# Kernel optimization log

Hardware: AMD Instinct MI355X
Metric: run time of the kernel (lower is better)

The kernel has to match this reference:

```python
import jax, jax.numpy as jnp
import numpy as np

N_ENT = 40000
N_REL2 = 500      # num_rel * 2
E_DIR = 200000
E_2HOP = 50000
D_IN = 128        # entity/relation init dim
D_EMB = 256       # embed_dim
N_HEADS = 4
N_HID = D_EMB // N_HEADS  # 64
LRELU_ALPHA = 0.2
BN_EPS = 1e-5


def setup_inputs() -> dict:
    key = jax.random.key(0)
    ks = jax.random.split(key, 13)
    s = 0.1  # weight init scale
    return {
        "edge_index": jax.random.randint(ks[0], (2, E_DIR), 0, N_ENT),
        "edge_type": jax.random.randint(ks[1], (E_DIR,), 0, N_REL2),
        "indices_2hop": jax.random.randint(ks[2], (E_2HOP, 4), 0, N_REL2),
        "init_embed": jax.random.normal(ks[3], (N_ENT, D_IN), jnp.float32) * s,
        "init_rel": jax.random.normal(ks[4], (N_REL2, D_IN), jnp.float32) * s,
        "W_heads": jax.random.normal(ks[5], (N_HEADS, 2 * D_IN + D_IN, N_HID), jnp.float32) * s,
        "a_heads": jax.random.normal(ks[6], (N_HEADS, N_HID, 1), jnp.float32) * s,
        "gat_W": jax.random.normal(ks[7], (D_IN, D_EMB), jnp.float32) * s,
        "out_W": jax.random.normal(ks[8], (2 * D_EMB + D_EMB, D_EMB), jnp.float32) * s,
        "out_a": jax.random.normal(ks[9], (D_EMB, 1), jnp.float32) * s,
        "W_entities": jax.random.normal(ks[10], (D_IN, D_EMB), jnp.float32) * s,
        "bn_gamma": jnp.ones((D_EMB,), jnp.float32),
        "bn_beta": jnp.zeros((D_EMB,), jnp.float32),
    }


def segment_softmax(logits, idx, num_seg):
    # sparse softmax grouped by idx (PyG-style): subtract per-segment max, exp, normalize
    m = jax.ops.segment_max(logits, idx, num_segments=num_seg)
    e = jnp.exp(logits - m[idx])
    s = jax.ops.segment_sum(e, idx, num_segments=num_seg)
    return e / (s[idx] + 1e-16)


def reference(edge_index, edge_type, indices_2hop, init_embed, init_rel,
              W_heads, a_heads, gat_W, out_W, out_a, W_entities, bn_gamma, bn_beta):
    n = init_embed.shape[0]
    # build full edge list: flipped direct edges + 2-hop edges
    edge_nhop = jnp.stack([indices_2hop[:, 3], indices_2hop[:, 0]])  # [2, E2]
    ei = jnp.concatenate([edge_index[::-1], edge_nhop], axis=1)      # [2, Etot]
    row, col = ei[0], ei[1]
    t0, t1 = indices_2hop[:, 1], indices_2hop[:, 2]

    # first-layer edge relation embeddings
    edge_embed = jnp.concatenate([init_rel[edge_type], init_rel[t0] + init_rel[t1]], axis=0)
    feat = jnp.concatenate([init_embed[row], init_embed[col], edge_embed], axis=1)  # [Etot, 3*D_IN]

    def head(W, a):
        eh = feat @ W                                     # [Etot, N_HID]
        logit = jax.nn.leaky_relu((eh @ a)[:, 0], LRELU_ALPHA)
        alpha = segment_softmax(logit, row, n)
        agg = jax.ops.segment_sum(alpha[:, None] * eh, row, num_segments=n)
        return jax.nn.elu(agg)                            # concat=True -> elu

    x = jax.vmap(head)(W_heads, a_heads)                  # [H, N, N_HID]
    x = jnp.transpose(x, (1, 0, 2)).reshape(n, -1)        # [N, H*N_HID]

    r = init_rel @ gat_W                                  # [R2, D_EMB]
    edge_embed2 = jnp.concatenate([r[edge_type], r[t0] + r[t1]], axis=0)
    feat2 = jnp.concatenate([x[row], x[col], edge_embed2], axis=1)  # [Etot, 3*D_EMB]
    eh2 = feat2 @ out_W                                   # [Etot, D_EMB]
    logit2 = jax.nn.leaky_relu((eh2 @ out_a)[:, 0], LRELU_ALPHA)
    alpha2 = segment_softmax(logit2, row, n)
    out = jax.ops.segment_sum(alpha2[:, None] * eh2, row, num_segments=n)
    x = jax.nn.elu(out)                                   # elu applied in GAT.forward

    x = x + init_embed @ W_entities
    # BatchNorm1d (training-mode batch stats, biased variance)
    mu = jnp.mean(x, axis=0)
    var = jnp.var(x, axis=0)
    x = (x - mu) / jnp.sqrt(var + BN_EPS) * bn_gamma + bn_beta
    return x, r
```

## Files before the change

kernel.cpp:

```cpp
#include <hip/hip_runtime.h>
#include <hip/hip_bf16.h>
#include <math.h>

#define N_ENT 40000
#define N_REL 500
#define E_DIR 200000
#define E_2HOP 50000
#define E_TOT 250000
#define D_IN 128
#define D_EMB 256
#define LRELU 0.2f
#define BN_EPS 1e-5f
#define NB_SCAN 157
#define NB_EDGE 977
#define N_HEAVY 500
#define DEG_SPLIT 32

typedef __hip_bfloat16 bf16;
typedef __attribute__((ext_vector_type(8))) short short8;
typedef __attribute__((ext_vector_type(4))) float float4v;

__device__ __forceinline__ float b2f(bf16 v){ return __bfloat162float(v); }
__device__ __forceinline__ float bitsf(unsigned int u){ return __builtin_bit_cast(float, u); }
__device__ __forceinline__ unsigned short bbits(float v){ return __builtin_bit_cast(unsigned short, __float2bfloat16(v)); }

__device__ __forceinline__ int e_row(int e, const int* ei, const int* i2){
  return (e < E_DIR) ? ei[E_DIR + e] : i2[(e - E_DIR)*4 + 3];
}

__global__ void prep_hist(const float* __restrict__ Wh, const float* __restrict__ ow,
                          const float* __restrict__ we, const float* __restrict__ emb,
                          bf16* __restrict__ WAp, bf16* __restrict__ WBp, bf16* __restrict__ WEp,
                          bf16* __restrict__ OWp0, bf16* __restrict__ OWp1, float* __restrict__ WC,
                          bf16* __restrict__ embb,
                          const int* __restrict__ ei, const int* __restrict__ i2, int* __restrict__ cnt){
  const int HS = 384*64;
  int b = blockIdx.x, tid = threadIdx.x;
  if (b < NB_EDGE){
    int e = b*256 + tid;
    if (e < E_TOT) atomicAdd(&cnt[e_row(e, ei, i2)], 1);
    return;
  }
  b -= NB_EDGE;
  if (b >= 240){
    int i = (b - 240)*256 + tid;
    embb[i] = __float2bfloat16(emb[i]);
    return;
  }
  if (b < 112){
    int seg, base;
    if      (b < 16){ seg = 0; base = 0; }
    else if (b < 32){ seg = 1; base = 16; }
    else if (b < 48){ seg = 2; base = 32; }
    else if (b < 80){ seg = 3; base = 48; }
    else            { seg = 4; base = 80; }
    int idx = (b - base)*256 + tid;
    int lane = idx & 63, nt = (idx >> 6) & 15, kc = idx >> 10;
    int quad = lane >> 4, l16 = lane & 15;
    int col = nt*16 + l16;
    int kbase = kc*32 + quad*8;
    bf16* dst = (seg==0?WAp : seg==1?WBp : seg==2?WEp : seg==3?OWp0 : OWp1) + (size_t)idx*8;
    #pragma unroll
    for (int j = 0; j < 8; j++){
      int k = kbase + j;
      float v;
      if      (seg == 0) v = Wh[(col>>6)*HS + k*64 + (col&63)];
      else if (seg == 1) v = Wh[(col>>6)*HS + (k+128)*64 + (col&63)];
      else if (seg == 2) v = we[(size_t)k*256 + col];
      else if (seg == 3) v = ow[(size_t)k*256 + col];
      else               v = ow[(size_t)(k+256)*256 + col];
      dst[j] = __float2bfloat16(v);
    }
  } else {
    int idx = (b - 112)*256 + tid;
    int k = idx >> 8, col = idx & 255;
    WC[idx] = Wh[(col>>6)*HS + (k+256)*64 + (col&63)];
  }
}

__global__ void scan_bsum(const int* __restrict__ cnt, int* __restrict__ bsum){
  int i = blockIdx.x*256 + threadIdx.x;
  int v = (i < N_ENT) ? cnt[i] : 0;
  int lane = threadIdx.x & 63, w = threadIdx.x >> 6;
  int s = v;
  #pragma unroll
  for (int o = 32; o >= 1; o >>= 1) s += __shfl_xor(s, o, 64);
  __shared__ int ws[4];
  if (lane == 0) ws[w] = s;
  __syncthreads();
  if (threadIdx.x == 0) bsum[blockIdx.x] = ws[0]+ws[1]+ws[2]+ws[3];
}

__global__ __launch_bounds__(256) void scan_final2(const int* __restrict__ cnt,
    const int* __restrict__ bsum, int* __restrict__ off){
  __shared__ int boffs[NB_SCAN];
  __shared__ int ws4[4];
  __shared__ int ws2[4];
  __shared__ int totals;
  int t = threadIdx.x;
  int lane = t & 63, w = t >> 6;
  {
    int v = (t < NB_SCAN) ? bsum[t] : 0;
    int s = v;
    #pragma unroll
    for (int o = 1; o < 64; o <<= 1){ int n = __shfl_up(s, o, 64); if (lane >= o) s += n; }
    if (lane == 63) ws4[w] = s;
    __syncthreads();
    int add = 0;
    for (int k = 0; k < w; k++) add += ws4[k];
    int incl = s + add;
    if (t < NB_SCAN) boffs[t] = incl - v;
    if (t == NB_SCAN-1) totals = incl;
  }
  __syncthreads();
  int i = blockIdx.x*256 + t;
  int v = (i < N_ENT) ? cnt[i] : 0;
  int s = v;
  #pragma unroll
  for (int o = 1; o < 64; o <<= 1){ int n = __shfl_up(s, o, 64); if (lane >= o) s += n; }
  if (lane == 63) ws2[w] = s;
  __syncthreads();
  int add = boffs[blockIdx.x];
  for (int k = 0; k < w; k++) add += ws2[k];
  if (i < N_ENT) off[i] = add + s - v;
  if (blockIdx.x == 0 && t == 0) off[N_ENT] = totals;
}

__device__ __forceinline__ void mfma_panel(const short* __restrict__ A,
    const short* __restrict__ Bp, bf16* __restrict__ C, int K,
    const float* __restrict__ avec, float* __restrict__ Sout, int dmode,
    int bx, int half){
  int w = threadIdx.x >> 6, lane = threadIdx.x & 63;
  int quad = lane >> 4, l16 = lane & 15;
  int rm = bx*64 + w*16;
  int arow = rm + l16;
  float4v acc[8];
  #pragma unroll
  for (int nt = 0; nt < 8; nt++) acc[nt] = (float4v){0.f,0.f,0.f,0.f};
  int nkc = K >> 5;
  const short8* Ap = (const short8*)(A + (size_t)arow*K);
  const short8* Bv = (const short8*)Bp + half*512 + lane;
  short8 a_cur = Ap[quad];
  for (int kc = 0; kc < nkc; kc++){
    int kn = (kc + 1 < nkc) ? kc + 1 : kc;
    short8 a_nxt = Ap[kn*4 + quad];
    const short8* bp = Bv + (size_t)kc*1024;
    short8 b[4];
    #pragma unroll
    for (int nt = 0; nt < 4; nt++) b[nt] = bp[nt*64];
    #pragma unroll
    for (int nt = 0; nt < 4; nt++)
      acc[nt] = __builtin_amdgcn_mfma_f32_16x16x32_bf16(a_cur, b[nt], acc[nt], 0, 0, 0);
    #pragma unroll
    for (int nt = 0; nt < 4; nt++) b[nt] = bp[(nt+4)*64];
    #pragma unroll
    for (int nt = 0; nt < 4; nt++)
      acc[nt+4] = __builtin_amdgcn_mfma_f32_16x16x32_bf16(a_cur, b[nt], acc[nt+4], 0, 0, 0);
    a_cur = a_nxt;
  }
  #pragma unroll
  for (int nt = 0; nt < 8; nt++){
    int col = (half*8 + nt)*16 + l16;
    #pragma unroll
    for (int r = 0; r < 4; r++)
      C[(size_t)(rm + quad*4 + r)*256 + col] = __float2bfloat16(acc[nt][r]);
  }
  if (Sout){
    if (dmode == 0){
      #pragma unroll
      for (int hl = 0; hl < 2; hl++){
        float pr[4] = {0.f,0.f,0.f,0.f};
        #pragma unroll
        for (int ntl = 0; ntl < 4; ntl++){
          int ln = hl*4 + ntl;
          float av = avec[(half*8 + ln)*16 + l16];
          #pragma unroll
          for (int r = 0; r < 4; r++) pr[r] += acc[ln][r]*av;
        }
        #pragma unroll
        for (int m = 8; m >= 1; m >>= 1)
          #pragma unroll
          for (int r = 0; r < 4; r++) pr[r] += __shfl_xor(pr[r], m, 64);
        if (l16 == 0){
          #pragma unroll
          for (int r = 0; r < 4; r++)
            Sout[(rm + quad*4 + r)*4 + half*2 + hl] = pr[r];
        }
      }
    } else {
      float pr[4] = {0.f,0.f,0.f,0.f};
      #pragma unroll
      for (int ln = 0; ln < 8; ln++){
        float av = avec[(half*8 + ln)*16 + l16];
        #pragma unroll
        for (int r = 0; r < 4; r++) pr[r] += acc[ln][r]*av;
      }
      #pragma unroll
      for (int m = 8; m >= 1; m >>= 1)
        #pragma unroll
        for (int r = 0; r < 4; r++) pr[r] += __shfl_xor(pr[r], m, 64);
      if (l16 == 0){
        #pragma unroll
        for (int r = 0; r < 4; r++) atomicAdd(&Sout[rm + quad*4 + r], pr[r]);
      }
    }
  }
}

__device__ __forceinline__ void gemm64_body(const float* __restrict__ A,
    const float* __restrict__ B, float* __restrict__ C, bf16* __restrict__ Cb,
    int M, int K, const float* __restrict__ av, float* __restrict__ So, int mode,
    int bxx, int byy, char* smem){
  const int N = 256;
  float (*As)[65] = (float (*)[65])smem;
  float (*Bsf)[65] = (float (*)[65])(smem + 16*65*sizeof(float));
  int bm = bxx * 64, bn = byy * 64;
  int tid = threadIdx.x;
  int tx = tid & 15, ty = tid >> 4;
  float acc[4][4] = {};
  for (int k0 = 0; k0 < K; k0 += 16){
    #pragma unroll
    for (int j = 0; j < 4; j++){
      int idx = tid + j*256;
      int m = idx >> 4, kk = idx & 15;
      int gm = bm + m;
      float v = 0.f;
      if (gm < M) v = A[(size_t)gm*K + k0 + kk];
      As[kk][m] = v;
    }
    #pragma unroll
    for (int j = 0; j < 4; j++){
      int idx = tid + j*256;
      int kk = idx >> 6, n = idx & 63;
      Bsf[kk][n] = B[(size_t)(k0+kk)*N + bn + n];
    }
    __syncthreads();
    #pragma unroll
    for (int kk = 0; kk < 16; kk++){
      float a[4], b[4];
      #pragma unroll
      for (int i = 0; i < 4; i++) a[i] = As[kk][ty*4+i];
      #pragma unroll
      for (int j = 0; j < 4; j++) b[j] = Bsf[kk][tx*4+j];
      #pragma unroll
      for (int i = 0; i < 4; i++)
        #pragma unroll
        for (int j = 0; j < 4; j++) acc[i][j] += a[i]*b[j];
    }
    __syncthreads();
  }
  if (Cb){
    #pragma unroll
    for (int i = 0; i < 4; i++){
      int gm = bm + ty*4 + i;
      if (gm >= M) continue;
      #pragma unroll
      for (int j = 0; j < 4; j++)
        Cb[(size_t)gm*N + bn + tx*4 + j] = __float2bfloat16(acc[i][j]);
    }
  } else {
    #pragma unroll
    for (int i = 0; i < 4; i++){
      int gm = bm + ty*4 + i;
      if (gm >= M) continue;
      #pragma unroll
      for (int j = 0; j < 4; j++)
        C[(size_t)gm*N + bn + tx*4 + j] = acc[i][j];
    }
  }
  if (mode != 2){
    float pr[4];
    #pragma unroll
    for (int i = 0; i < 4; i++){
      float p = 0.f;
      #pragma unroll
      for (int j = 0; j < 4; j++) p += acc[i][j]*av[bn + tx*4 + j];
      pr[i] = p;
    }
    #pragma unroll
    for (int m = 8; m >= 1; m >>= 1)
      #pragma unroll
      for (int i = 0; i < 4; i++) pr[i] += __shfl_xor(pr[i], m, 64);
    if (tx == 0){
      #pragma unroll
      for (int i = 0; i < 4; i++){
        int gm = bm + ty*4 + i;
        if (gm < M){
          if (mode == 0) So[gm*4 + byy] = pr[i];
          else atomicAdd(&So[gm], pr[i]);
        }
      }
    }
  }
}

__device__ __forceinline__ void scatter_body(const int* __restrict__ ei, const int* __restrict__ et,
    const int* __restrict__ i2, const int* __restrict__ off,
    int* __restrict__ cur, int4* __restrict__ EIDX, int blk){
  int e = blk*256 + threadIdx.x;
  if (e >= E_TOT) return;
  int r = e_row(e, ei, i2);
  int p = atomicAdd(&cur[r], 1);
  int d = off[r] + p;
  int4 v;
  if (e < E_DIR){ v.x = ei[e]; v.y = et[e]; v.z = -1; }
  else { int q = (e - E_DIR)*4; v.x = i2[q]; v.y = i2[q+1]; v.z = i2[q+2]; }
  v.w = r;
  EIDX[d] = v;
}

__global__ __launch_bounds__(256, 4) void mega1(
    const short* __restrict__ embb, const short* __restrict__ WAp, const short* __restrict__ WBp,
    const short* __restrict__ WEp, bf16* __restrict__ P1, bf16* __restrict__ P2, bf16* __restrict__ EP,
    const float* __restrict__ ah, float* __restrict__ S1, float* __restrict__ S2,
    const float* __restrict__ rel, const float* __restrict__ WC, const float* __restrict__ gw,
    float* __restrict__ RF, float* __restrict__ SRm, bf16* __restrict__ PRb,
    const int* __restrict__ ei, const int* __restrict__ et, const int* __restrict__ i2,
    const int* __restrict__ off, int* __restrict__ cur, int4* __restrict__ EIDX, int useEP){
  __shared__ char smem[8704];
  int y = blockIdx.y, x = blockIdx.x;
  if (x < 1250){
    if (y == 2 && !useEP) return;
    const short* B = y==0 ? WAp : (y==1 ? WBp : WEp);
    bf16* C = y==0 ? P1 : (y==1 ? P2 : EP);
    float* S = y==0 ? S1 : (y==1 ? S2 : nullptr);
    mfma_panel(embb, B, C, 128, ah, S, 0, x >> 1, x & 1);
    return;
  }
  int r = x - 1250;
  if (y == 0){
    if (r < 64){
      int z = r >> 5, rr = r & 31, by = rr >> 3, bx = rr & 7;
      if (z == 0) gemm64_body(rel, WC, nullptr, PRb, N_REL, 128, ah, SRm, 0, bx, by, smem);
      else        gemm64_body(rel, gw, RF, nullptr, N_REL, 128, nullptr, nullptr, 2, bx, by, smem);
    }
  } else if (y == 1){
    if (r < NB_EDGE) scatter_body(ei, et, i2, off, cur, EIDX, r);
  }
}

__global__ __launch_bounds__(256, 4) void mega2(
    const short* __restrict__ X1s, const short* __restrict__ OWp0, const short* __restrict__ OWp1,
    bf16* __restrict__ Q1, bf16* __restrict__ Q2, const float* __restrict__ oa,
    float* __restrict__ S1B, float* __restrict__ S2B,
    const float* __restrict__ RF, const float* __restrict__ owB, float* __restrict__ SRB,
    bf16* __restrict__ QRb){
  __shared__ char smem[8704];
  int y = blockIdx.y, x = blockIdx.x;
  if (x < 1250){
    mfma_panel(X1s, y==0 ? OWp0 : OWp1, y==0 ? Q1 : Q2, 256, oa,
               y==0 ? S1B : S2B, 1, x >> 1, x & 1);
    return;
  }
  int r = x - 1250;
  if (y == 0 && r < 32){
    int by = r >> 3, bx = r & 7;
    gemm64_body(RF, owB, nullptr, QRb, N_REL, 256, oa, SRB, 1, bx, by, smem);
  }
}

__global__ void gemm64_acc(const float* __restrict__ A, const float* __restrict__ B,
                           float* __restrict__ C, int M, int K){
  const int N = 256;
  __shared__ float As[16][65];
  __shared__ float Bs[16][65];
  int bm = blockIdx.x * 64, bn = blockIdx.y * 64;
  int tid = threadIdx.x;
  int tx = tid & 15, ty = tid >> 4;
  float acc[4][4] = {};
  for (int k0 = 0; k0 < K; k0 += 16){
    #pragma unroll
    for (int j = 0; j < 4; j++){
      int idx = tid + j*256;
      int m = idx >> 4, kk = idx & 15;
      int gm = bm + m;
      float v = 0.f;
      if (gm < M) v = A[(size_t)gm*K + k0 + kk];
      As[kk][m] = v;
    }
    #pragma unroll
    for (int j = 0; j < 4; j++){
      int idx = tid + j*256;
      int kk = idx >> 6, n = idx & 63;
      Bs[kk][n] = B[(size_t)(k0+kk)*N + bn + n];
    }
    __syncthreads();
    #pragma unroll
    for (int kk = 0; kk < 16; kk++){
      float a[4], b[4];
      #pragma unroll
      for (int i = 0; i < 4; i++) a[i] = As[kk][ty*4+i];
      #pragma unroll
      for (int j = 0; j < 4; j++) b[j] = Bs[kk][tx*4+j];
      #pragma unroll
      for (int i = 0; i < 4; i++)
        #pragma unroll
        for (int j = 0; j < 4; j++) acc[i][j] += a[i]*b[j];
    }
    __syncthreads();
  }
  #pragma unroll
  for (int i = 0; i < 4; i++){
    int gm = bm + ty*4 + i;
    if (gm >= M) continue;
    #pragma unroll
    for (int j = 0; j < 4; j++){
      size_t o = (size_t)gm*N + bn + tx*4 + j;
      C[o] += acc[i][j];
    }
  }
}

__global__ __launch_bounds__(256) void sm1f(const int* __restrict__ off, const int4* __restrict__ EIDX,
    const float* __restrict__ s1, const float* __restrict__ s2, const float* __restrict__ sR,
    float* __restrict__ L1, float* __restrict__ AS1, float* __restrict__ IV1){
  if (blockIdx.x < N_HEAVY){
    int i = blockIdx.x;
    int st = off[i], en = off[i+1];
    if (en - st <= DEG_SPLIT) return;
    int h = threadIdx.x >> 6, lane = threadIdx.x & 63;
    float* Lh = L1 + (size_t)h*E_TOT;
    float si = s1[i*4 + h];
    float mx = -1e30f;
    for (int t = st + lane; t < en; t += 64){
      int4 e = EIDX[t];
      float v = si + s2[e.x*4+h] + sR[e.y*4+h];
      if (e.z >= 0) v += sR[e.z*4+h];
      v = (v >= 0.f) ? v : LRELU*v;
      Lh[t] = v;
      mx = fmaxf(mx, v);
    }
    #pragma unroll
    for (int o = 32; o >= 1; o >>= 1) mx = fmaxf(mx, __shfl_xor(mx, o, 64));
    float sm = 0.f;
    for (int t = st + lane; t < en; t += 64){
      float ev = __expf(Lh[t] - mx); Lh[t] = ev; sm += ev;
    }
    #pragma unroll
    for (int o = 32; o >= 1; o >>= 1) sm += __shfl_xor(sm, o, 64);
    float inv = 1.f/(sm + 1e-16f);
    if (lane == 0){ AS1[i*4+h] = sm*inv; IV1[i*4+h] = inv; }
    return;
  }
  int wid = threadIdx.x >> 6, lane = threadIdx.x & 63;
  int i = (blockIdx.x - N_HEAVY)*4 + wid;
  if (i >= N_ENT) return;
  int st = off[i], en = off[i+1];
  if (i < N_HEAVY && en - st > DEG_SPLIT) return;
  int hf = lane >> 4, l16 = lane & 15;
  float* Lh = L1 + (size_t)hf*E_TOT;
  float si = s1[i*4 + hf];
  if (en - st > 2*16){
    float mx = -1e30f;
    for (int t = st + l16; t < en; t += 16){
      int4 e = EIDX[t];
      float v = si + s2[e.x*4+hf] + sR[e.y*4+hf];
      if (e.z >= 0) v += sR[e.z*4+hf];
      v = (v >= 0.f) ? v : LRELU*v;
      Lh[t] = v; mx = fmaxf(mx, v);
    }
    #pragma unroll
    for (int o = 8; o >= 1; o >>= 1) mx = fmaxf(mx, __shfl_xor(mx, o, 64));
    float sm = 0.f;
    for (int t = st + l16; t < en; t += 16){
      float ev = __expf(Lh[t] - mx); Lh[t] = ev; sm += ev;
    }
    #pragma unroll
    for (int o = 8; o >= 1; o >>= 1) sm += __shfl_xor(sm, o, 64);
    float inv = 1.f/(sm + 1e-16f);
    if (l16 == 0){ AS1[i*4+hf] = sm*inv; IV1[i*4+hf] = inv; }
    return;
  }
  int t0 = st + l16, t1 = t0 + 16;
  float v0 = -1e30f, v1 = -1e30f;
  if (t0 < en){
    int4 e = EIDX[t0];
    float v = si + s2[e.x*4+hf] + sR[e.y*4+hf];
    if (e.z >= 0) v += sR[e.z*4+hf];
    v0 = (v >= 0.f) ? v : LRELU*v;
  }
  if (t1 < en){
    int4 e = EIDX[t1];
    float v = si + s2[e.x*4+hf] + sR[e.y*4+hf];
    if (e.z >= 0) v += sR[e.z*4+hf];
    v1 = (v >= 0.f) ? v : LRELU*v;
  }
  float mx = fmaxf(v0, v1);
  #pragma unroll
  for (int o = 8; o >= 1; o >>= 1) mx = fmaxf(mx, __shfl_xor(mx, o, 64));
  float sm = 0.f;
  if (t0 < en){ float ev = __expf(v0 - mx); Lh[t0] = ev; sm += ev; }
  if (t1 < en){ float ev = __expf(v1 - mx); Lh[t1] = ev; sm += ev; }
  #pragma unroll
  for (int o = 8; o >= 1; o >>= 1) sm += __shfl_xor(sm, o, 64);
  float inv = 1.f/(sm + 1e-16f);
  if (l16 == 0){ AS1[i*4+hf] = sm*inv; IV1[i*4+hf] = inv; }
}

__global__ __launch_bounds__(256) void sm2f(const int* __restrict__ off, const int4* __restrict__ EIDX,
    const float* __restrict__ s1, const float* __restrict__ s2, const float* __restrict__ sR,
    float* __restrict__ L2, float* __restrict__ AS2, float* __restrict__ IV2){
  __shared__ float wsm[4], wss[4];
  if (blockIdx.x < N_HEAVY){
    int i = blockIdx.x;
    int st = off[i], en = off[i+1];
    if (en - st <= DEG_SPLIT) return;
    int tid = threadIdx.x, w = tid >> 6, lane = tid & 63;
    float si = s1[i];
    float mx = -1e30f;
    for (int t = st + tid; t < en; t += 256){
      int4 e = EIDX[t];
// ... 304 lines not shown
  int wid = threadIdx.x >> 6, lane = threadIdx.x & 63;
  int i = (blockIdx.x - N_HEAVY)*4 + wid;
  if (i >= N_ENT) return;
  int st = off[i], en = off[i+1];
  if (i < N_HEAVY && en - st > DEG_SPLIT) return;
  int f0 = lane*4;
  size_t ob = (size_t)i*256 + f0;
  float ep0=0.f, ep1=0.f, ep2=0.f, ep3=0.f;
  if (EP){
    uint2 ue = *(const uint2*)(EP + ob);
    ep0 = bitsf(ue.x << 16); ep1 = bitsf(ue.x & 0xffff0000u);
    ep2 = bitsf(ue.y << 16); ep3 = bitsf(ue.y & 0xffff0000u);
  }
  if (st == en){
    *(float4*)(X2 + ob) = (float4){ep0, ep1, ep2, ep3};
    return;
  }
  float a0=0,a1=0,a2=0,a3=0;
  int t = st;
  int n4 = st + ((en - st) & ~3);
  for (; t < n4; t += 4){
    int4 e[4]; float wv[4]; uint2 u[4]; uint2 rr[4];
    #pragma unroll
    for (int k = 0; k < 4; k++){ e[k] = EIDX[t+k]; wv[k] = W2[t+k]; }
    #pragma unroll
    for (int k = 0; k < 4; k++){
      u[k] = *(const uint2*)(Q2 + (size_t)e[k].x*256 + f0);
      rr[k] = *(const uint2*)(QRm + (size_t)e[k].y*256 + f0);
    }
    float rf[4][4];
    #pragma unroll
    for (int k = 0; k < 4; k++){ UNPK(rr[k], rf[k][0], rf[k][1], rf[k][2], rf[k][3]) }
    #pragma unroll
    for (int k = 0; k < 4; k++){
      if (e[k].z >= 0){
        uint2 s = *(const uint2*)(QRm + (size_t)e[k].z*256 + f0);
        float s0,s1,s2,s3; UNPK(s, s0,s1,s2,s3)
        rf[k][0] += s0; rf[k][1] += s1; rf[k][2] += s2; rf[k][3] += s3;
      }
    }
    #pragma unroll
    for (int k = 0; k < 4; k++){
      a0 += wv[k]*(bitsf(u[k].x << 16) + rf[k][0]);
      a1 += wv[k]*(bitsf(u[k].x & 0xffff0000u) + rf[k][1]);
      a2 += wv[k]*(bitsf(u[k].y << 16) + rf[k][2]);
      a3 += wv[k]*(bitsf(u[k].y & 0xffff0000u) + rf[k][3]);
    }
  }
  for (; t < en; t++){
    float w = W2[t];
    int4 e = EIDX[t];
    uint2 u = *(const uint2*)(Q2 + (size_t)e.x*256 + f0);
    uint2 rr = *(const uint2*)(QRm + (size_t)e.y*256 + f0);
    float r0,r1,r2,r3; UNPK(rr, r0,r1,r2,r3)
    if (e.z >= 0){
      uint2 s = *(const uint2*)(QRm + (size_t)e.z*256 + f0);
      float s0,s1,s2,s3; UNPK(s, s0,s1,s2,s3)
      r0 += s0; r1 += s1; r2 += s2; r3 += s3;
    }
    a0 += w*(bitsf(u.x << 16) + r0);
    a1 += w*(bitsf(u.x & 0xffff0000u) + r1);
    a2 += w*(bitsf(u.y << 16) + r2);
    a3 += w*(bitsf(u.y & 0xffff0000u) + r3);
  }
  float iv = IV2[i];
  a0 *= iv; a1 *= iv; a2 *= iv; a3 *= iv;
  float as = AS2[i];
  uint2 uq = *(const uint2*)(Q1 + ob);
  a0 += as*bitsf(uq.x << 16);
  a1 += as*bitsf(uq.x & 0xffff0000u);
  a2 += as*bitsf(uq.y << 16);
  a3 += as*bitsf(uq.y & 0xffff0000u);
  a0 = ((a0 > 0.f) ? a0 : __expf(a0)-1.f) + ep0;
  a1 = ((a1 > 0.f) ? a1 : __expf(a1)-1.f) + ep1;
  a2 = ((a2 > 0.f) ? a2 : __expf(a2)-1.f) + ep2;
  a3 = ((a3 > 0.f) ? a3 : __expf(a3)-1.f) + ep3;
  *(float4*)(X2 + ob) = (float4){a0, a1, a2, a3};
}

__global__ void bn_reduce(const float* __restrict__ X, float* __restrict__ sums, float* __restrict__ sq){
  int ch = threadIdx.x;
  float s = 0.f, q = 0.f;
  for (int r = blockIdx.x; r < N_ENT; r += gridDim.x){
    float v = X[(size_t)r*256 + ch];
    s += v; q += v*v;
  }
  atomicAdd(&sums[ch], s);
  atomicAdd(&sq[ch], q);
}

__global__ void bn_final_r(float* __restrict__ X, const float* __restrict__ sums, const float* __restrict__ sq,
                           const float* __restrict__ gamma, const float* __restrict__ beta,
                           const float* __restrict__ RF, float* __restrict__ out_r){
  int b = blockIdx.x;
  if (b < 40000){
    int idx = b*256 + threadIdx.x;
    int ch = idx & 255;
    const float invn = 1.f/(float)N_ENT;
    float mean = sums[ch] * invn;
    float var  = fmaxf(sq[ch] * invn - mean*mean, 0.f);
    X[idx] = (X[idx] - mean) * rsqrtf(var + BN_EPS) * gamma[ch] + beta[ch];
  } else {
    int idx = (b - 40000)*256 + threadIdx.x;
    out_r[idx] = RF[idx];
  }
}

extern "C" void kernel_launch(void* const* d_in, const int* in_sizes, int n_in,
                              void* d_out, int out_size, void* d_ws, size_t ws_size,
                              hipStream_t stream){
  const int*   ei  = (const int*)d_in[0];
  const int*   et  = (const int*)d_in[1];
  const int*   i2  = (const int*)d_in[2];
  const float* emb = (const float*)d_in[3];
  const float* rel = (const float*)d_in[4];
  const float* Wh  = (const float*)d_in[5];
  const float* ah  = (const float*)d_in[6];
  const float* gw  = (const float*)d_in[7];
  const float* ow  = (const float*)d_in[8];
  const float* oa  = (const float*)d_in[9];
  const float* we  = (const float*)d_in[10];
  const float* gma = (const float*)d_in[11];
  const float* bta = (const float*)d_in[12];
  float* out = (float*)d_out;

  char* ws = (char*)d_ws;
  size_t o = 0;
  auto alloc = [&](size_t bytes)->char*{
    char* p = ws + o; o = (o + bytes + 255) & ~(size_t)255; return p;
  };
  bf16*  P1  = (bf16*)alloc(20480000);
  bf16*  P2  = (bf16*)alloc(20480000);
  bf16*  PRb = (bf16*)alloc(256000);
  bf16*  QRb = (bf16*)alloc(256000);
  float* RF  = (float*)alloc(512000);
  float* WC  = (float*)alloc(131072);
  bf16*  WAp = (bf16*)alloc(65536);
  bf16*  WBp = (bf16*)alloc(65536);
  bf16*  WEp = (bf16*)alloc(65536);
  bf16*  OWp0= (bf16*)alloc(131072);
  bf16*  OWp1= (bf16*)alloc(131072);
  float* S1  = (float*)alloc(640000);
  float* S2  = (float*)alloc(640000);
  float* SRm = (float*)alloc(8192);
  float* S1B = (float*)alloc(160000);
  float* S2B = (float*)alloc(160000);
  int*   CNT = (int*)alloc(160000);
  int*   CUR = (int*)alloc(160000);
  float* SRB = (float*)alloc(2048);
  float* BNS = (float*)alloc(1024);
  float* BNQ = (float*)alloc(1024);
  int*   OFF = (int*)alloc(160016);
  int*   BSUM= (int*)alloc(1024);
  int4*  EIDX= (int4*)alloc(4000000);
  float* L1  = (float*)alloc(4000000);
  float* L2  = (float*)alloc(1000000);
  float* AS1 = (float*)alloc(640000);
  float* AS2 = (float*)alloc(160000);
  float* IV1 = (float*)alloc(640000);
  float* IV2 = (float*)alloc(160000);
  size_t base_end = o;
  bool useEP = (ws_size >= base_end + 20480256 + 512);
  bf16* EP = nullptr;
  if (useEP) EP = (bf16*)alloc(20480000);
  bf16* X1b  = (bf16*)out;
  bf16* embb = (bf16*)((char*)out + 20480000);
  float* X2 = out;
  (void)in_sizes; (void)n_in; (void)out_size;

  hipMemsetAsync(S1B, 0, 644096, stream);

  prep_hist<<<NB_EDGE + 20240, 256, 0, stream>>>(Wh, ow, we, emb,
      WAp, WBp, WEp, OWp0, OWp1, WC, embb, ei, i2, CNT);

  scan_bsum<<<NB_SCAN, 256, 0, stream>>>(CNT, BSUM);
  scan_final2<<<NB_SCAN, 256, 0, stream>>>(CNT, BSUM, OFF);

  mega1<<<dim3(1250 + NB_EDGE, 3), 256, 0, stream>>>(
      (const short*)embb, (const short*)WAp, (const short*)WBp, (const short*)WEp,
      P1, P2, EP, ah, S1, S2,
      rel, WC, gw, RF, SRm, PRb,
      ei, et, i2, OFF, CUR, EIDX, useEP ? 1 : 0);

  sm1f<<<N_HEAVY + N_ENT/4, 256, 0, stream>>>(OFF, EIDX, S1, S2, SRm, L1, AS1, IV1);
  agg1<<<N_HEAVY + N_ENT/4, 256, 0, stream>>>(OFF, EIDX, L1, AS1, IV1, P1, P2, PRb, X1b);

  mega2<<<dim3(1250 + 32, 2), 256, 0, stream>>>(
      (const short*)X1b, (const short*)OWp0, (const short*)OWp1,
      P1, P2, oa, S1B, S2B, RF, ow + 131072, SRB, QRb);

  sm2f<<<N_HEAVY + N_ENT/4, 256, 0, stream>>>(OFF, EIDX, S1B, S2B, SRB, L2, AS2, IV2);
  agg2<<<N_HEAVY + N_ENT/4, 256, 0, stream>>>(OFF, EIDX, L2, AS2, IV2, P1, P2, QRb, EP, X2);

  if (!useEP)
    gemm64_acc<<<dim3((N_ENT+63)/64, 4), 256, 0, stream>>>(emb, we, X2, N_ENT, 128);

  bn_reduce<<<1024, 256, 0, stream>>>(X2, BNS, BNQ);
  bn_final_r<<<40500, 256, 0, stream>>>(X2, BNS, BNQ, gma, bta, RF, out + (size_t)N_ENT*256);
}
```

Before: 401.3 us.

## Make MFMA GEMM panels persistent with weight slices staged in LDS

Replaces the per-tile MFMA panel with a persistent kernel body. Each block loads its weight column slice into 32KB of shared memory once, using global_load_lds, then loops over row tiles with a stride, so B is no longer re-read from global memory for every tile. The launch grids of mega1 and mega2 are flattened to 1D and the column split is regrouped: mega2 now uses 4 quarter-width slices with K=256. The larger LDS footprint lowers achievable occupancy, and A rows are still streamed from global memory.

Result: slower. 463.5 us (+15.5%).

```diff
diff --git a/kernel.cpp b/kernel.cpp
--- a/kernel.cpp
+++ b/kernel.cpp
@@ -15,6 +15,9 @@
 #define NB_EDGE 977
 #define N_HEAVY 500
 #define DEG_SPLIT 32
+#define N_TILES 625
+#define BPU1 208
+#define BPU2 160
 
 typedef __hip_bfloat16 bf16;
 typedef __attribute__((ext_vector_type(8))) short short8;
@@ -23,6 +26,12 @@
 __device__ __forceinline__ float b2f(bf16 v){ return __bfloat162float(v); }
 __device__ __forceinline__ float bitsf(unsigned int u){ return __builtin_bit_cast(float, u); }
 __device__ __forceinline__ unsigned short bbits(float v){ return __builtin_bit_cast(unsigned short, __float2bfloat16(v)); }
+
+typedef const __attribute__((address_space(1))) void* gptr_t;
+typedef __attribute__((address_space(3))) void* lptr_t;
+__device__ __forceinline__ void gload_lds16(const void* g, void* l){
+  __builtin_amdgcn_global_load_lds((gptr_t)g, (lptr_t)l, 16, 0, 0);
+}
 
 __device__ __forceinline__ int e_row(int e, const int* ei, const int* i2){
   return (e < E_DIR) ? ei[E_DIR + e] : i2[(e - E_DIR)*4 + 3];
@@ -126,56 +135,99 @@
   if (blockIdx.x == 0 && t == 0) off[N_ENT] = totals;
 }
 
-__device__ __forceinline__ void mfma_panel(const short* __restrict__ A,
-    const short* __restrict__ Bp, bf16* __restrict__ C, int K,
+template<int NKC, int NTL>
+__device__ __forceinline__ void mfma_persist(const short* __restrict__ A,
+    const short* __restrict__ Bp, bf16* __restrict__ C,
     const float* __restrict__ avec, float* __restrict__ Sout, int dmode,
-    int bx, int half){
-  int w = threadIdx.x >> 6, lane = threadIdx.x & 63;
+    int nt0, int tile0, int stride, char* smem){
+  const int CPB8 = NTL*64;
+  int tid = threadIdx.x, w = tid >> 6, lane = tid & 63;
   int quad = lane >> 4, l16 = lane & 15;
-  int rm = bx*64 + w*16;
-  int arow = rm + l16;
-  float4v acc[8];
-  #pragma unroll
-  for (int nt = 0; nt < 8; nt++) acc[nt] = (float4v){0.f,0.f,0.f,0.f};
-  int nkc = K >> 5;
-  const short8* Ap = (const short8*)(A + (size_t)arow*K);
-  const short8* Bv = (const short8*)Bp + half*512 + lane;
-  short8 a_cur = Ap[quad];
-  for (int kc = 0; kc < nkc; kc++){
-    int kn = (kc + 1 < nkc) ? kc + 1 : kc;
-    short8 a_nxt = Ap[kn*4 + quad];
-    const short8* bp = Bv + (size_t)kc*1024;
-    short8 b[4];
-    #pragma unroll
-    for (int nt = 0; nt < 4; nt++) b[nt] = bp[nt*64];
-    #pragma unroll
-    for (int nt = 0; nt < 4; nt++)
-      acc[nt] = __builtin_amdgcn_mfma_f32_16x16x32_bf16(a_cur, b[nt], acc[nt], 0, 0, 0);
-    #pragma unroll
-    for (int nt = 0; nt < 4; nt++) b[nt] = bp[(nt+4)*64];
-    #pragma unroll
-    for (int nt = 0; nt < 4; nt++)
-      acc[nt+4] = __builtin_amdgcn_mfma_f32_16x16x32_bf16(a_cur, b[nt], acc[nt+4], 0, 0, 0);
-    a_cur = a_nxt;
-  }
-  #pragma unroll
-  for (int nt = 0; nt < 8; nt++){
-    int col = (half*8 + nt)*16 + l16;
-    #pragma unroll
-    for (int r = 0; r < 4; r++)
-      C[(size_t)(rm + quad*4 + r)*256 + col] = __float2bfloat16(acc[nt][r]);
-  }
-  if (Sout){
-    if (dmode == 0){
-      #pragma unroll
-      for (int hl = 0; hl < 2; hl++){
+  {
+    const short8* Bv = (const short8*)Bp;
+    short8* Bw = (short8*)smem;
+    #pragma unroll
+    for (int kc = 0; kc < NKC; kc++){
+      #pragma unroll
+      for (int s = 0; s < CPB8; s += 256){
+        int dstBase = kc*CPB8 + s + w*64;
+        size_t srcBase = (size_t)kc*1024 + nt0*64 + s + w*64;
+        gload_lds16((const void*)(Bv + srcBase + lane), (void*)(Bw + dstBase));
+      }
+    }
+  }
+  __syncthreads();
+  const short8* Bs = (const short8*)smem;
+  for (int t = tile0; t < N_TILES; t += stride){
+    int rm = t*64 + w*16;
+    int arow = rm + l16;
+    const short8* Ap = (const short8*)(A + (size_t)arow*(NKC*32));
+    short8 a[NKC];
+    #pragma unroll
+    for (int kc = 0; kc < NKC; kc++) a[kc] = Ap[kc*4 + quad];
+    float4v acc[NTL];
+    #pragma unroll
+    for (int n = 0; n < NTL; n++) acc[n] = (float4v){0.f,0.f,0.f,0.f};
+    #pragma unroll
+    for (int kc = 0; kc < NKC; kc++){
+      const short8* bp = Bs + kc*CPB8 + lane;
+      if (NTL == 8){
+        short8 b[4];
+        #pragma unroll
+        for (int n = 0; n < 4; n++) b[n] = bp[n*64];
+        #pragma unroll
+        for (int n = 0; n < 4; n++)
+          acc[n] = __builtin_amdgcn_mfma_f32_16x16x32_bf16(a[kc], b[n], acc[n], 0, 0, 0);
+        #pragma unroll
+        for (int n = 0; n < 4; n++) b[n] = bp[(n+4)*64];
+        #pragma unroll
+        for (int n = 0; n < 4; n++)
+          acc[n+4] = __builtin_amdgcn_mfma_f32_16x16x32_bf16(a[kc], b[n], acc[n+4], 0, 0, 0);
+      } else {
+        short8 b[NTL];
+        #pragma unroll
+        for (int n = 0; n < NTL; n++) b[n] = bp[n*64];
+        #pragma unroll
+        for (int n = 0; n < NTL; n++)
+          acc[n] = __builtin_amdgcn_mfma_f32_16x16x32_bf16(a[kc], b[n], acc[n], 0, 0, 0);
+      }
+    }
+    #pragma unroll
+    for (int n = 0; n < NTL; n++){
+      int col = (nt0 + n)*16 + l16;
+      #pragma unroll
+      for (int r = 0; r < 4; r++)
+        C[(size_t)(rm + quad*4 + r)*256 + col] = __float2bfloat16(acc[n][r]);
+    }
+    if (Sout){
+      if (dmode == 0){
+        #pragma unroll
+        for (int hl = 0; hl < 2; hl++){
+          float pr[4] = {0.f,0.f,0.f,0.f};
+          #pragma unroll
+          for (int n = 0; n < 4; n++){
+            float av = avec[(nt0 + hl*4 + n)*16 + l16];
+            #pragma unroll
+            for (int r = 0; r < 4; r++) pr[r] += acc[hl*4+n][r]*av;
+          }
+          #pragma unroll
+          for (int m = 8; m >= 1; m >>= 1)
+            #pragma unroll
+            for (int r = 0; r < 4; r++) pr[r] += __shfl_xor(pr[r], m, 64);
+          if (l16 == 0){
+            int head = (nt0 >> 2) + hl;
+            #pragma unroll
+            for (int r = 0; r < 4; r++)
+              Sout[(rm + quad*4 + r)*4 + head] = pr[r];
+          }
+        }
+      } else {
         float pr[4] = {0.f,0.f,0.f,0.f};
         #pragma unroll
-        for (int ntl = 0; ntl < 4; ntl++){
-          int ln = hl*4 + ntl;
-          float av = avec[(half*8 + ln)*16 + l16];
+        for (int n = 0; n < NTL; n++){
+          float av = avec[(nt0 + n)*16 + l16];
           #pragma unroll
-          for (int r = 0; r < 4; r++) pr[r] += acc[ln][r]*av;
+          for (int r = 0; r < 4; r++) pr[r] += acc[n][r]*av;
         }
         #pragma unroll
         for (int m = 8; m >= 1; m >>= 1)
@@ -183,25 +235,8 @@
           for (int r = 0; r < 4; r++) pr[r] += __shfl_xor(pr[r], m, 64);
         if (l16 == 0){
           #pragma unroll
-          for (int r = 0; r < 4; r++)
-            Sout[(rm + quad*4 + r)*4 + half*2 + hl] = pr[r];
+          for (int r = 0; r < 4; r++) atomicAdd(&Sout[rm + quad*4 + r], pr[r]);
         }
-      }
-    } else {
-      float pr[4] = {0.f,0.f,0.f,0.f};
-      #pragma unroll
-      for (int ln = 0; ln < 8; ln++){
-        float av = avec[(half*8 + ln)*16 + l16];
-        #pragma unroll
-        for (int r = 0; r < 4; r++) pr[r] += acc[ln][r]*av;
-      }
-      #pragma unroll
-      for (int m = 8; m >= 1; m >>= 1)
-        #pragma unroll
-        for (int r = 0; r < 4; r++) pr[r] += __shfl_xor(pr[r], m, 64);
-      if (l16 == 0){
-        #pragma unroll
-        for (int r = 0; r < 4; r++) atomicAdd(&Sout[rm + quad*4 + r], pr[r]);
       }
     }
   }
@@ -317,26 +352,27 @@
     float* __restrict__ RF, float* __restrict__ SRm, bf16* __restrict__ PRb,
     const int* __restrict__ ei, const int* __restrict__ et, const int* __restrict__ i2,
     const int* __restrict__ off, int* __restrict__ cur, int4* __restrict__ EIDX, int useEP){
-  __shared__ char smem[8704];
-  int y = blockIdx.y, x = blockIdx.x;
-  if (x < 1250){
-    if (y == 2 && !useEP) return;
-    const short* B = y==0 ? WAp : (y==1 ? WBp : WEp);
-    bf16* C = y==0 ? P1 : (y==1 ? P2 : EP);
-    float* S = y==0 ? S1 : (y==1 ? S2 : nullptr);
-    mfma_panel(embb, B, C, 128, ah, S, 0, x >> 1, x & 1);
-    return;
-  }
-  int r = x - 1250;
-  if (y == 0){
-    if (r < 64){
-      int z = r >> 5, rr = r & 31, by = rr >> 3, bx = rr & 7;
-      if (z == 0) gemm64_body(rel, WC, nullptr, PRb, N_REL, 128, ah, SRm, 0, bx, by, smem);
-      else        gemm64_body(rel, gw, RF, nullptr, N_REL, 128, nullptr, nullptr, 2, bx, by, smem);
-    }
-  } else if (y == 1){
-    if (r < NB_EDGE) scatter_body(ei, et, i2, off, cur, EIDX, r);
-  }
+  __shared__ char smem[32768];
+  int x = blockIdx.x;
+  if (x < 6*BPU1){
+    int u = x / BPU1;
+    int p = u >> 1, half = u & 1;
+    if (p == 2 && !useEP) return;
+    const short* B = p==0 ? WAp : (p==1 ? WBp : WEp);
+    bf16* C = p==0 ? P1 : (p==1 ? P2 : EP);
+    float* S = p==0 ? S1 : (p==1 ? S2 : nullptr);
+    mfma_persist<4,8>(embb, B, C, ah, S, 0, half*8, x % BPU1, BPU1, smem);
+    return;
+  }
+  int r = x - 6*BPU1;
+  if (r < 64){
+    int z = r >> 5, rr = r & 31, by = rr >> 3, bx = rr & 7;
+    if (z == 0) gemm64_body(rel, WC, nullptr, PRb, N_REL, 128, ah, SRm, 0, bx, by, smem);
+    else        gemm64_body(rel, gw, RF, nullptr, N_REL, 128, nullptr, nullptr, 2, bx, by, smem);
+    return;
+  }
+  r -= 64;
+  if (r < NB_EDGE) scatter_body(ei, et, i2, off, cur, EIDX, r);
 }
 
 __global__ __launch_bounds__(256, 4) void mega2(
@@ -345,15 +381,17 @@
     float* __restrict__ S1B, float* __restrict__ S2B,
     const float* __restrict__ RF, const float* __restrict__ owB, float* __restrict__ SRB,
     bf16* __restrict__ QRb){
-  __shared__ char smem[8704];
-  int y = blockIdx.y, x = blockIdx.x;
-  if (x < 1250){
-    mfma_panel(X1s, y==0 ? OWp0 : OWp1, y==0 ? Q1 : Q2, 256, oa,
-               y==0 ? S1B : S2B, 1, x >> 1, x & 1);
-    return;
-  }
-  int r = x - 1250;
-  if (y == 0 && r < 32){
+  __shared__ char smem[32768];
+  int x = blockIdx.x;
+  if (x < 8*BPU2){
+    int u = x / BPU2;
+    int p = u >> 2, q = u & 3;
+    mfma_persist<8,4>(X1s, p==0 ? OWp0 : OWp1, p==0 ? Q1 : Q2, oa,
+                      p==0 ? S1B : S2B, 1, q*4, x % BPU2, BPU2, smem);
+    return;
+  }
+  int r = x - 8*BPU2;
+  if (r < 32){
     int by = r >> 3, bx = r & 7;
     gemm64_body(RF, owB, nullptr, QRb, N_REL, 256, oa, SRB, 1, bx, by, smem);
   }
@@ -991,7 +1029,7 @@
   scan_bsum<<<NB_SCAN, 256, 0, stream>>>(CNT, BSUM);
   scan_final2<<<NB_SCAN, 256, 0, stream>>>(CNT, BSUM, OFF);
 
-  mega1<<<dim3(1250 + NB_EDGE, 3), 256, 0, stream>>>(
+  mega1<<<6*BPU1 + 64 + NB_EDGE, 256, 0, stream>>>(
       (const short*)embb, (const short*)WAp, (const short*)WBp, (const short*)WEp,
       P1, P2, EP, ah, S1, S2,
       rel, WC, gw, RF, SRm, PRb,
@@ -1000,7 +1038,7 @@
   sm1f<<<N_HEAVY + N_ENT/4, 256, 0, stream>>>(OFF, EIDX, S1, S2, SRm, L1, AS1, IV1);
   agg1<<<N_HEAVY + N_ENT/4, 256, 0, stream>>>(OFF, EIDX, L1, AS1, IV1, P1, P2, PRb, X1b);
 
-  mega2<<<dim3(1250 + 32, 2), 256, 0, stream>>>(
+  mega2<<<8*BPU2 + 32, 256, 0, stream>>>(
       (const short*)X1b, (const short*)OWp0, (const short*)OWp1,
       P1, P2, oa, S1B, S2B, RF, ow + 131072, SRB, QRb);
 
```

## Build 2-hop CSR with per-block shared-memory histograms and reorder mega-kernel blocks

Applied to the files above, without the earlier changes.

The 2-hop edges all target rows below 500, so global atomics on those few counters are heavily contended. This change counts them with shared-memory histograms in 8 blocks and combines the partial counts with a small prefix-scan kernel. The scatter step then places each 2-hop edge at a precomputed slot filled from the end of each row's segment, instead of using global atomics. The mega kernels move to 1D grids with the scatter and small GEMM blocks scheduled first, which adds one tiny extra launch.

Result: faster. 373.9 us (-6.8%).

```diff
diff --git a/kernel.cpp b/kernel.cpp
--- a/kernel.cpp
+++ b/kernel.cpp
@@ -12,7 +12,9 @@
 #define LRELU 0.2f
 #define BN_EPS 1e-5f
 #define NB_SCAN 157
-#define NB_EDGE 977
+#define NB_DIR 782
+#define NB2 8
+#define E2PB 6250
 #define N_HEAVY 500
 #define DEG_SPLIT 32
 
@@ -23,25 +25,39 @@
 __device__ __forceinline__ float b2f(bf16 v){ return __bfloat162float(v); }
 __device__ __forceinline__ float bitsf(unsigned int u){ return __builtin_bit_cast(float, u); }
 __device__ __forceinline__ unsigned short bbits(float v){ return __builtin_bit_cast(unsigned short, __float2bfloat16(v)); }
-
-__device__ __forceinline__ int e_row(int e, const int* ei, const int* i2){
-  return (e < E_DIR) ? ei[E_DIR + e] : i2[(e - E_DIR)*4 + 3];
-}
 
 __global__ void prep_hist(const float* __restrict__ Wh, const float* __restrict__ ow,
                           const float* __restrict__ we, const float* __restrict__ emb,
                           bf16* __restrict__ WAp, bf16* __restrict__ WBp, bf16* __restrict__ WEp,
                           bf16* __restrict__ OWp0, bf16* __restrict__ OWp1, float* __restrict__ WC,
                           bf16* __restrict__ embb,
-                          const int* __restrict__ ei, const int* __restrict__ i2, int* __restrict__ cnt){
+                          const int* __restrict__ ei, const int* __restrict__ i2,
+                          int* __restrict__ cnt, int* __restrict__ H2){
+  __shared__ int hc[512];
   const int HS = 384*64;
   int b = blockIdx.x, tid = threadIdx.x;
-  if (b < NB_EDGE){
+  if (b < NB_DIR){
     int e = b*256 + tid;
-    if (e < E_TOT) atomicAdd(&cnt[e_row(e, ei, i2)], 1);
-    return;
-  }
-  b -= NB_EDGE;
+    if (e < E_DIR) atomicAdd(&cnt[ei[E_DIR + e]], 1);
+    return;
+  }
+  b -= NB_DIR;
+  if (b < NB2){
+    hc[tid] = 0; hc[tid + 256] = 0;
+    __syncthreads();
+    int base = b*E2PB;
+    for (int it = 0; it < 25; it++){
+      int o2 = it*256 + tid;
+      if (o2 < E2PB){
+        int r = i2[(base + o2)*4 + 3];
+        atomicAdd(&hc[r], 1);
+      }
+    }
+    __syncthreads();
+    for (int r = tid; r < 500; r += 256) H2[b*500 + r] = hc[r];
+    return;
+  }
+  b -= NB2;
   if (b >= 240){
     int i = (b - 240)*256 + tid;
     embb[i] = __float2bfloat16(emb[i]);
@@ -78,9 +94,21 @@
   }
 }
 
-__global__ void scan_bsum(const int* __restrict__ cnt, int* __restrict__ bsum){
+__global__ void h2scan(const int* __restrict__ H2, int* __restrict__ b2off, int* __restrict__ c2){
+  int r = threadIdx.x;
+  if (r < 500){
+    int s = 0;
+    #pragma unroll
+    for (int b = 0; b < NB2; b++){ b2off[b*500 + r] = s; s += H2[b*500 + r]; }
+    c2[r] = s;
+  }
+}
+
+__global__ void scan_bsum(const int* __restrict__ cnt, const int* __restrict__ c2,
+                          int* __restrict__ bsum){
   int i = blockIdx.x*256 + threadIdx.x;
-  int v = (i < N_ENT) ? cnt[i] : 0;
+  int v = 0;
+  if (i < N_ENT){ v = cnt[i]; if (i < 500) v += c2[i]; }
   int lane = threadIdx.x & 63, w = threadIdx.x >> 6;
   int s = v;
   #pragma unroll
@@ -92,7 +120,7 @@
 }
 
 __global__ __launch_bounds__(256) void scan_final2(const int* __restrict__ cnt,
-    const int* __restrict__ bsum, int* __restrict__ off){
+    const int* __restrict__ c2, const int* __restrict__ bsum, int* __restrict__ off){
   __shared__ int boffs[NB_SCAN];
   __shared__ int ws4[4];
   __shared__ int ws2[4];
@@ -114,7 +142,8 @@
   }
   __syncthreads();
   int i = blockIdx.x*256 + t;
-  int v = (i < N_ENT) ? cnt[i] : 0;
+  int v = 0;
+  if (i < N_ENT){ v = cnt[i]; if (i < 500) v += c2[i]; }
   int s = v;
   #pragma unroll
   for (int o = 1; o < 64; o <<= 1){ int n = __shfl_up(s, o, 64); if (lane >= o) s += n; }
@@ -294,21 +323,6 @@
   }
 }
 
-__device__ __forceinline__ void scatter_body(const int* __restrict__ ei, const int* __restrict__ et,
-    const int* __restrict__ i2, const int* __restrict__ off,
-    int* __restrict__ cur, int4* __restrict__ EIDX, int blk){
-  int e = blk*256 + threadIdx.x;
-  if (e >= E_TOT) return;
-  int r = e_row(e, ei, i2);
-  int p = atomicAdd(&cur[r], 1);
-  int d = off[r] + p;
-  int4 v;
-  if (e < E_DIR){ v.x = ei[e]; v.y = et[e]; v.z = -1; }
-  else { int q = (e - E_DIR)*4; v.x = i2[q]; v.y = i2[q+1]; v.z = i2[q+2]; }
-  v.w = r;
-  EIDX[d] = v;
-}
-
 __global__ __launch_bounds__(256, 4) void mega1(
     const short* __restrict__ embb, const short* __restrict__ WAp, const short* __restrict__ WBp,
     const short* __restrict__ WEp, bf16* __restrict__ P1, bf16* __restrict__ P2, bf16* __restrict__ EP,
@@ -316,27 +330,54 @@
     const float* __restrict__ rel, const float* __restrict__ WC, const float* __restrict__ gw,
     float* __restrict__ RF, float* __restrict__ SRm, bf16* __restrict__ PRb,
     const int* __restrict__ ei, const int* __restrict__ et, const int* __restrict__ i2,
-    const int* __restrict__ off, int* __restrict__ cur, int4* __restrict__ EIDX, int useEP){
+    const int* __restrict__ off, int* __restrict__ cur, const int* __restrict__ b2off,
+    int4* __restrict__ EIDX, int useEP){
   __shared__ char smem[8704];
-  int y = blockIdx.y, x = blockIdx.x;
-  if (x < 1250){
-    if (y == 2 && !useEP) return;
-    const short* B = y==0 ? WAp : (y==1 ? WBp : WEp);
-    bf16* C = y==0 ? P1 : (y==1 ? P2 : EP);
-    float* S = y==0 ? S1 : (y==1 ? S2 : nullptr);
-    mfma_panel(embb, B, C, 128, ah, S, 0, x >> 1, x & 1);
-    return;
-  }
-  int r = x - 1250;
-  if (y == 0){
-    if (r < 64){
-      int z = r >> 5, rr = r & 31, by = rr >> 3, bx = rr & 7;
-      if (z == 0) gemm64_body(rel, WC, nullptr, PRb, N_REL, 128, ah, SRm, 0, bx, by, smem);
-      else        gemm64_body(rel, gw, RF, nullptr, N_REL, 128, nullptr, nullptr, 2, bx, by, smem);
-    }
-  } else if (y == 1){
-    if (r < NB_EDGE) scatter_body(ei, et, i2, off, cur, EIDX, r);
-  }
+  __shared__ int lc[512];
+  int x = blockIdx.x, tid = threadIdx.x;
+  if (x < NB_DIR){
+    int e = x*256 + tid;
+    if (e < E_DIR){
+      int r = ei[E_DIR + e];
+      int p = atomicAdd(&cur[r], 1);
+      int4 v; v.x = ei[e]; v.y = et[e]; v.z = -1; v.w = r;
+      EIDX[off[r] + p] = v;
+    }
+    return;
+  }
+  x -= NB_DIR;
+  if (x < NB2){
+    lc[tid] = 0; lc[tid + 256] = 0;
+    __syncthreads();
+    int base = x*E2PB;
+    for (int it = 0; it < 25; it++){
+      int o2 = it*256 + tid;
+      if (o2 < E2PB){
+        int e2 = base + o2;
+        int q = e2*4;
+        int r = i2[q + 3];
+        int myp = atomicAdd(&lc[r], 1);
+        int d = off[r+1] - 1 - (b2off[x*500 + r] + myp);
+        int4 v; v.x = i2[q]; v.y = i2[q+1]; v.z = i2[q+2]; v.w = r;
+        EIDX[d] = v;
+      }
+    }
+    return;
+  }
+  x -= NB2;
+  if (x < 64){
+    int z = x >> 5, rr = x & 31, by = rr >> 3, bx = rr & 7;
+    if (z == 0) gemm64_body(rel, WC, nullptr, PRb, N_REL, 128, ah, SRm, 0, bx, by, smem);
+    else        gemm64_body(rel, gw, RF, nullptr, N_REL, 128, nullptr, nullptr, 2, bx, by, smem);
+    return;
+  }
+  x -= 64;
+  int p = x / 1250, rest = x % 1250;
+  if (p == 2 && !useEP) return;
+  const short* B = p==0 ? WAp : (p==1 ? WBp : WEp);
+  bf16* C = p==0 ? P1 : (p==1 ? P2 : EP);
+  float* S = p==0 ? S1 : (p==1 ? S2 : nullptr);
+  mfma_panel(embb, B, C, 128, ah, S, 0, rest >> 1, rest & 1);
 }
 
 __global__ __launch_bounds__(256, 4) void mega2(
@@ -346,17 +387,16 @@
     const float* __restrict__ RF, const float* __restrict__ owB, float* __restrict__ SRB,
     bf16* __restrict__ QRb){
   __shared__ char smem[8704];
-  int y = blockIdx.y, x = blockIdx.x;
-  if (x < 1250){
-    mfma_panel(X1s, y==0 ? OWp0 : OWp1, y==0 ? Q1 : Q2, 256, oa,
-               y==0 ? S1B : S2B, 1, x >> 1, x & 1);
-    return;
-  }
-  int r = x - 1250;
-  if (y == 0 && r < 32){
-    int by = r >> 3, bx = r & 7;
+  int x = blockIdx.x;
+  if (x < 32){
+    int by = x >> 3, bx = x & 7;
     gemm64_body(RF, owB, nullptr, QRb, N_REL, 256, oa, SRB, 1, bx, by, smem);
-  }
+    return;
+  }
+  x -= 32;
+  int p = x / 1250, rest = x % 1250;
+  mfma_panel(X1s, p==0 ? OWp0 : OWp1, p==0 ? Q1 : Q2, 256, oa,
+             p==0 ? S1B : S2B, 1, rest >> 1, rest & 1);
 }
 
 __global__ void gemm64_acc(const float* __restrict__ A, const float* __restrict__ B,
@@ -967,6 +1007,9 @@
   float* BNQ = (float*)alloc(1024);
   int*   OFF = (int*)alloc(160016);
   int*   BSUM= (int*)alloc(1024);
+  int*   H2  = (int*)alloc(16000);
+  int*   B2O = (int*)alloc(16000);
+  int*   C2  = (int*)alloc(2048);
   int4*  EIDX= (int4*)alloc(4000000);
   float* L1  = (float*)alloc(4000000);
   float* L2  = (float*)alloc(1000000);
@@ -985,22 +1028,23 @@
 
   hipMemsetAsync(S1B, 0, 644096, stream);
 
-  prep_hist<<<NB_EDGE + 20240, 256, 0, stream>>>(Wh, ow, we, emb,
-      WAp, WBp, WEp, OWp0, OWp1, WC, embb, ei, i2, CNT);
-
-  scan_bsum<<<NB_SCAN, 256, 0, stream>>>(CNT, BSUM);
-  scan_final2<<<NB_SCAN, 256, 0, stream>>>(CNT, BSUM, OFF);
-
-  mega1<<<dim3(1250 + NB_EDGE, 3), 256, 0, stream>>>(
+  prep_hist<<<NB_DIR + NB2 + 20240, 256, 0, stream>>>(Wh, ow, we, emb,
+      WAp, WBp, WEp, OWp0, OWp1, WC, embb, ei, i2, CNT, H2);
+
+  h2scan<<<1, 512, 0, stream>>>(H2, B2O, C2);
+  scan_bsum<<<NB_SCAN, 256, 0, stream>>>(CNT, C2, BSUM);
+  scan_final2<<<NB_SCAN, 256, 0, stream>>>(CNT, C2, BSUM, OFF);
+
+  mega1<<<NB_DIR + NB2 + 64 + 3750, 256, 0, stream>>>(
       (const short*)embb, (const short*)WAp, (const short*)WBp, (const short*)WEp,
       P1, P2, EP, ah, S1, S2,
       rel, WC, gw, RF, SRm, PRb,
-      ei, et, i2, OFF, CUR, EIDX, useEP ? 1 : 0);
+      ei, et, i2, OFF, CUR, B2O, EIDX, useEP ? 1 : 0);
 
   sm1f<<<N_HEAVY + N_ENT/4, 256, 0, stream>>>(OFF, EIDX, S1, S2, SRm, L1, AS1, IV1);
   agg1<<<N_HEAVY + N_ENT/4, 256, 0, stream>>>(OFF, EIDX, L1, AS1, IV1, P1, P2, PRb, X1b);
 
-  mega2<<<dim3(1250 + 32, 2), 256, 0, stream>>>(
+  mega2<<<32 + 2500, 256, 0, stream>>>(
       (const short*)X1b, (const short*)OWp0, (const short*)OWp1,
       P1, P2, oa, S1B, S2B, RF, ow + 131072, SRB, QRb);
 
```
